# Performance work log

Hardware: AMD Instinct MI355X
Metric: run time of the kernel (lower is better)

## Reference

```python
import jax, jax.numpy as jnp
import numpy as np

GROUPS = 32
EPS = 1e-5
N_HEADS = 4


def group_norm(x, w, b):
    # x: [B, C, T]; GroupNorm over (C/G, T) within each of G groups
    B, C, T = x.shape
    xg = x.reshape(B, GROUPS, (C // GROUPS) * T)
    mean = xg.mean(axis=-1, keepdims=True)
    var = xg.var(axis=-1, keepdims=True)
    xn = ((xg - mean) * jax.lax.rsqrt(var + EPS)).reshape(B, C, T)
    return xn * w[None, :, None] + b[None, :, None]


def setup_inputs() -> dict:
    key = jax.random.key(0)
    ks = jax.random.split(key, 5)
    B, C, H, W = 2, 256, 64, 64
    x = jax.random.normal(ks[0], (B, C, H, W), dtype=jnp.float32)
    norm_w = jnp.ones((C,), dtype=jnp.float32)
    norm_b = jnp.zeros((C,), dtype=jnp.float32)
    qkv_w = jax.random.normal(ks[1], (3 * C, C), dtype=jnp.float32) * (C ** -0.5)
    qkv_b = jax.random.normal(ks[2], (3 * C,), dtype=jnp.float32) * 0.02
    proj_w = jax.random.normal(ks[3], (C, C), dtype=jnp.float32) * (C ** -0.5)
    proj_b = jax.random.normal(ks[4], (C,), dtype=jnp.float32) * 0.02
    return {"x": x, "norm_w": norm_w, "norm_b": norm_b,
            "qkv_w": qkv_w, "qkv_b": qkv_b,
            "proj_w": proj_w, "proj_b": proj_b}


def reference(x, norm_w, norm_b, qkv_w, qkv_b, proj_w, proj_b):
    B, C, Hs, Ws = x.shape
    T = Hs * Ws
    xf = x.reshape(B, C, T)
    xn = group_norm(xf, norm_w, norm_b)
    # 1x1 conv1d == channel matmul: [3C,C] x [B,C,T] -> [B,3C,T]
    qkv = jnp.einsum('oc,bct->bot', qkv_w, xn) + qkv_b[None, :, None]
    ch = C // N_HEADS
    # legacy order: [B, H*3*ch, T] -> [B*H, 3*ch, T] -> split
    qkv_h = qkv.reshape(B * N_HEADS, 3 * ch, T)
    q, k, v = qkv_h[:, :ch], qkv_h[:, ch:2 * ch], qkv_h[:, 2 * ch:]
    scale = ch ** -0.25
    # full [B*H, T, T] score matrix, softmax in fp32 (faithful to source)
    weight = jnp.einsum('bct,bcs->bts', q * scale, k * scale)
    weight = jax.nn.softmax(weight.astype(jnp.float32), axis=-1).astype(qkv.dtype)
    a = jnp.einsum('bts,bcs->bct', weight, v).reshape(B, C, T)
    h = jnp.einsum('oc,bct->bot', proj_w, a) + proj_b[None, :, None]
    return (xf + h).reshape(B, C, Hs, Ws)
```

## Files before the change

kernel.cpp:

```cpp
#include <hip/hip_runtime.h>
#include <hip/hip_bf16.h>

#define B_    2
#define C_    256
#define T_    4096
#define GRP   32
#define CPG   8
#define NH    4
#define CH    64
#define K3C   768
#define SPLIT 4
#define GSL   8
#define NSTAT (B_ * GRP * GSL)
#define NCVT  128
#define LOG2E 1.4426950408889634f

typedef __attribute__((ext_vector_type(8))) short bf16x8;
typedef __attribute__((ext_vector_type(4))) float f32x4;
typedef __attribute__((ext_vector_type(16))) float f32x16;

#if __has_builtin(__builtin_amdgcn_exp2f)
#define EXP2(x) __builtin_amdgcn_exp2f(x)
#else
#define EXP2(x) exp2f(x)
#endif

__device__ __forceinline__ unsigned pk2(float a, float b) {
    __hip_bfloat162 h = __float22bfloat162_rn(make_float2(a, b));
    union { __hip_bfloat162 h2; unsigned u; } cv; cv.h2 = h;
    return cv.u;
}
__device__ __forceinline__ float bf2f(unsigned short u) {
    return __uint_as_float((unsigned)u << 16);
}

__device__ __forceinline__ void gl_lds16(const unsigned short* g, unsigned short* l) {
    __builtin_amdgcn_global_load_lds(
        (const __attribute__((address_space(1))) unsigned int*)g,
        (__attribute__((address_space(3))) unsigned int*)l,
        16, 0, 0);
}

__global__ __launch_bounds__(256) void pre_kernel(
    const float* __restrict__ x, float* __restrict__ stat,
    const float* __restrict__ qw, const float* __restrict__ pw,
    unsigned short* __restrict__ qwb, unsigned short* __restrict__ pwb) {
    int bid = blockIdx.x;
    int tid = threadIdx.x;
    if (bid < NSTAT) {
        int bg = bid >> 3, sl = bid & 7;
        const int SLN = CPG * T_ / GSL;
        const float* xp = x + (size_t)bg * CPG * T_ + (size_t)sl * SLN;
        float s = 0.f, s2 = 0.f;
        for (int i = tid * 4; i < SLN; i += 1024) {
            float4 v = *(const float4*)&xp[i];
            s  += (v.x + v.y) + (v.z + v.w);
            s2 += (v.x * v.x + v.y * v.y) + (v.z * v.z + v.w * v.w);
        }
        for (int off = 32; off > 0; off >>= 1) {
            s  += __shfl_down(s,  off);
            s2 += __shfl_down(s2, off);
        }
        __shared__ float rs[4], rs2[4];
        int wid = tid >> 6;
        if ((tid & 63) == 0) { rs[wid] = s; rs2[wid] = s2; }
        __syncthreads();
        if (tid == 0) {
            stat[bid * 2]     = (rs[0] + rs[1]) + (rs[2] + rs[3]);
            stat[bid * 2 + 1] = (rs2[0] + rs2[1]) + (rs2[2] + rs2[3]);
        }
    } else {
        int i = (bid - NSTAT) * 256 + tid;
        const int n1 = K3C * C_ / 8;
        const float* src; unsigned short* dst;
        if (i < n1) { src = qw + 8 * i; dst = qwb + 8 * i; }
        else { int j = i - n1; src = pw + 8 * j; dst = pwb + 8 * j; }
        float4 a = *(const float4*)src;
        float4 b = *(const float4*)(src + 4);
        uint4 u;
        u.x = pk2(a.x, a.y); u.y = pk2(a.z, a.w);
        u.z = pk2(b.x, b.y); u.w = pk2(b.z, b.w);
        *(uint4*)dst = u;
    }
}

__global__ __launch_bounds__(256) void gn_apply_kernel(
    const float* __restrict__ x, const float* __restrict__ stat,
    const float* __restrict__ w, const float* __restrict__ b,
    unsigned short* __restrict__ xnT) {
    int bg = blockIdx.x, sl = blockIdx.y;
    int batch = bg / GRP, g = bg % GRP;
    const float* xp = x + (size_t)bg * CPG * T_;
    int tid = threadIdx.x;

    float s = 0.f, s2 = 0.f;
#pragma unroll
    for (int i = 0; i < GSL; ++i) {
        s  += stat[(bg * GSL + i) * 2];
        s2 += stat[(bg * GSL + i) * 2 + 1];
    }
    float inv_n = 1.f / (float)(CPG * T_);
    float mean = s * inv_n;
    float var  = s2 * inv_n - mean * mean;
    float inv  = rsqrtf(var + 1e-5f);

    float wv[8], bv[8];
#pragma unroll
    for (int j = 0; j < 8; j++) {
        float ww = w[g * CPG + j] * inv;
        wv[j] = ww;
        bv[j] = b[g * CPG + j] - mean * ww;
    }
    unsigned short* op = xnT + (size_t)batch * T_ * C_ + g * CPG;
    int t0 = sl * (T_ / GSL);
#pragma unroll
    for (int rep = 0; rep < 2; ++rep) {
        int t = t0 + rep * 256 + tid;
        float v[8];
#pragma unroll
        for (int j = 0; j < 8; j++) v[j] = xp[(size_t)j * T_ + t] * wv[j] + bv[j];
        uint4 u;
        u.x = pk2(v[0], v[1]); u.y = pk2(v[2], v[3]);
        u.z = pk2(v[4], v[5]); u.w = pk2(v[6], v[7]);
        *(uint4*)&op[(size_t)t * C_] = u;
    }
}

__global__ __launch_bounds__(256) void qkv_gemm_kernel(
    const unsigned short* __restrict__ Wb, const float* __restrict__ bias,
    const unsigned short* __restrict__ Xt, unsigned short* __restrict__ q_t,
    unsigned short* __restrict__ k_t, unsigned short* __restrict__ v_d) {
    int tb = blockIdx.x * 128;
    int by = blockIdx.y;
    int bz = blockIdx.z;
    int ob = by * 64;
    int tid = threadIdx.x;
    int l = tid & 15, oct = (tid >> 4) & 3, w = tid >> 6;

    __shared__ __align__(16) unsigned short SH[64 * 264];

#pragma unroll
    for (int j = 0; j < 8; ++j) {
        int idx = tid + 256 * j;
        int row = idx >> 5, ch = idx & 31;
        *(uint4*)&SH[row * 264 + ch * 8] =
            *(const uint4*)&Wb[(size_t)(ob + row) * C_ + ch * 8];
    }
    __syncthreads();

    const unsigned short* Xb = Xt + (size_t)bz * T_ * C_;

    f32x4 acc[4][2];
#pragma unroll
    for (int mf = 0; mf < 4; ++mf)
#pragma unroll
        for (int nf = 0; nf < 2; ++nf) acc[mf][nf] = (f32x4){0.f, 0.f, 0.f, 0.f};

#pragma unroll
    for (int kk = 0; kk < 8; ++kk) {
        int c0 = 32 * kk + 8 * oct;
        bf16x8 bfr[2];
#pragma unroll
        for (int nf = 0; nf < 2; ++nf)
            bfr[nf] = *(const bf16x8*)&Xb[(size_t)(tb + 32 * w + 16 * nf + l) * C_ + c0];
#pragma unroll
        for (int mf = 0; mf < 4; ++mf) {
            bf16x8 af = *(const bf16x8*)&SH[(16 * mf + l) * 264 + c0];
#pragma unroll
            for (int nf = 0; nf < 2; ++nf)
                acc[mf][nf] = __builtin_amdgcn_mfma_f32_16x16x32_bf16(af, bfr[nf], acc[mf][nf], 0, 0, 0);
        }
    }

    int head = by / 3, sec = by - 3 * head;
    int bh = bz * NH + head;

    if (sec < 2) {
        float scale = (sec == 0) ? 0.125f * LOG2E : 1.f;
        unsigned short* dst = ((sec == 0) ? q_t : k_t) + (size_t)bh * T_ * CH;
#pragma unroll
        for (int mf = 0; mf < 4; ++mf) {
            float bvs[4];
#pragma unroll
            for (int r = 0; r < 4; ++r) bvs[r] = bias[ob + 16 * mf + 4 * oct + r];
#pragma unroll
            for (int nf = 0; nf < 2; ++nf) {
                int t = tb + 32 * w + 16 * nf + l;
                float v0 = (acc[mf][nf][0] + bvs[0]) * scale;
                float v1 = (acc[mf][nf][1] + bvs[1]) * scale;
                float v2 = (acc[mf][nf][2] + bvs[2]) * scale;
                float v3 = (acc[mf][nf][3] + bvs[3]) * scale;
                uint2 u; u.x = pk2(v0, v1); u.y = pk2(v2, v3);
                *(uint2*)&dst[(size_t)t * CH + 16 * mf + 4 * oct] = u;
            }
        }
    } else {
        __syncthreads();
#pragma unroll
        for (int mf = 0; mf < 4; ++mf) {
            float bvs[4];
#pragma unroll
            for (int r = 0; r < 4; ++r) bvs[r] = bias[ob + 16 * mf + 4 * oct + r];
#pragma unroll
            for (int nf = 0; nf < 2; ++nf) {
                int tl = 32 * w + 16 * nf + l;
#pragma unroll
                for (int r = 0; r < 4; ++r) {
                    unsigned pv = pk2(acc[mf][nf][r] + bvs[r], 0.f);
                    SH[(16 * mf + 4 * oct + r) * 136 + tl] = (unsigned short)(pv & 0xffffu);
                }
            }
        }
        __syncthreads();
        unsigned short* vdst = v_d + (size_t)bh * CH * T_;
#pragma unroll
        for (int j = 0; j < 4; ++j) {
            int idx = tid + 256 * j;
            int row = idx >> 4, ch = idx & 15;
            *(uint4*)&vdst[(size_t)row * T_ + tb + ch * 8] =
                *(uint4*)&SH[row * 136 + ch * 8];
        }
    }
}

__global__ __launch_bounds__(256, 4) void attn_kernel(
    const unsigned short* __restrict__ q_t, const unsigned short* __restrict__ k_t,
    const unsigned short* __restrict__ v_d, unsigned short* __restrict__ Opart,
    float* __restrict__ lbuf) {
    int bh = blockIdx.y;
    int sp = blockIdx.z;
    int t0 = blockIdx.x * 128;
    int tid = threadIdx.x;
    int ln = tid & 63;
    int li = ln & 31;
    int hi = ln >> 5;
    int w  = tid >> 6;
    int l7 = li & 7;

    __shared__ __align__(16) unsigned short Kt[2][64 * 64];
    __shared__ __align__(16) unsigned short Vt[2][64 * 64];

    const unsigned short* qb = q_t + (size_t)bh * T_ * CH;
    const unsigned short* kb = k_t + (size_t)bh * T_ * CH;
    const unsigned short* vb = v_d + (size_t)bh * CH * T_;

    int tq = t0 + 32 * w + li;
    bf16x8 qf[4];
#pragma unroll
    for (int ks = 0; ks < 4; ++ks)
        qf[ks] = *(const bf16x8*)&qb[(size_t)tq * CH + ks * 16 + 8 * hi];

    int rsub = ln >> 3;
    int sch  = ln & 7;
    int cm8 = (sch ^ rsub) * 8;
    int kr0 = 16 * w + rsub;

#define STAGE(buf, s0) do {                                                          \
    gl_lds16(kb + (size_t)((s0) + kr0) * CH + cm8,     &Kt[buf][(16 * w) * 64]);     \
    gl_lds16(kb + (size_t)((s0) + kr0 + 8) * CH + cm8, &Kt[buf][(16 * w + 8) * 64]); \
    gl_lds16(vb + (size_t)kr0 * T_ + (s0) + cm8,       &Vt[buf][(16 * w) * 64]);     \
    gl_lds16(vb + (size_t)(kr0 + 8) * T_ + (s0) + cm8, &Vt[buf][(16 * w + 8) * 64]); \
} while (0)

    f32x16 O0, O1;
#pragma unroll
    for (int i = 0; i < 16; ++i) { O0[i] = 0.f; O1[i] = 0.f; }
    float l_run = 0.f;

    int s_beg = sp * (T_ / SPLIT);
    const int NT = (T_ / SPLIT) / 64;

    STAGE(0, s_beg);
    __syncthreads();

    int cur = 0;
    for (int t = 0; t < NT; ++t) {
        if (t + 1 < NT) STAGE(cur ^ 1, s_beg + (t + 1) * 64);

        f32x16 S0, S1;
#pragma unroll
        for (int i = 0; i < 16; ++i) { S0[i] = 0.f; S1[i] = 0.f; }
        __builtin_amdgcn_s_setprio(1);
#pragma unroll
        for (int ks = 0; ks < 4; ++ks) {
            bf16x8 ka0 = *(const bf16x8*)
                &Kt[cur][li * 64 + (((2 * ks + hi) ^ l7) * 8)];
            bf16x8 ka1 = *(const bf16x8*)
                &Kt[cur][(32 + li) * 64 + (((2 * ks + hi) ^ l7) * 8)];
            S0 = __builtin_amdgcn_mfma_f32_32x32x16_bf16(ka0, qf[ks], S0, 0, 0, 0);
            S1 = __builtin_amdgcn_mfma_f32_32x32x16_bf16(ka1, qf[ks], S1, 0, 0, 0);
        }
        __builtin_amdgcn_s_setprio(0);

        unsigned W0[8], W1[8];
        float lloc = 0.f;
#pragma unroll
        for (int h = 0; h < 4; ++h) {
            float a0 = EXP2(S0[4 * h + 0]), a1 = EXP2(S0[4 * h + 1]);
            float a2 = EXP2(S0[4 * h + 2]), a3 = EXP2(S0[4 * h + 3]);
            float b0 = EXP2(S1[4 * h + 0]), b1 = EXP2(S1[4 * h + 1]);
            float b2 = EXP2(S1[4 * h + 2]), b3 = EXP2(S1[4 * h + 3]);
            lloc += ((a0 + a1) + (a2 + a3)) + ((b0 + b1) + (b2 + b3));
            W0[2 * h] = pk2(a0, a1); W0[2 * h + 1] = pk2(a2, a3);
            W1[2 * h] = pk2(b0, b1); W1[2 * h + 1] = pk2(b2, b3);
        }
        l_run += lloc;

        __builtin_amdgcn_s_setprio(1);
#pragma unroll
        for (int g = 0; g < 4; ++g) {
            int ks = g & 1;
            unsigned w0, w1, w2, w3;
            if (g < 2) {
                w0 = W0[4 * ks + 0]; w1 = W0[4 * ks + 1];
                w2 = W0[4 * ks + 2]; w3 = W0[4 * ks + 3];
            } else {
                w0 = W1[4 * ks + 0]; w1 = W1[4 * ks + 1];
                w2 = W1[4 * ks + 2]; w3 = W1[4 * ks + 3];
            }
            asm("v_permlane32_swap_b32 %0, %1" : "+v"(w0), "+v"(w2));
            asm("v_permlane32_swap_b32 %0, %1" : "+v"(w1), "+v"(w3));
            union { unsigned u[4]; bf16x8 v; } pu;
            pu.u[0] = w0; pu.u[1] = w1; pu.u[2] = w2; pu.u[3] = w3;
            bf16x8 va0 = *(const bf16x8*)
                &Vt[cur][li * 64 + (((2 * g + hi) ^ l7) * 8)];
            bf16x8 va1 = *(const bf16x8*)
                &Vt[cur][(32 + li) * 64 + (((2 * g + hi) ^ l7) * 8)];
            O0 = __builtin_amdgcn_mfma_f32_32x32x16_bf16(va0, pu.v, O0, 0, 0, 0);
            O1 = __builtin_amdgcn_mfma_f32_32x32x16_bf16(va1, pu.v, O1, 0, 0, 0);
        }
        __builtin_amdgcn_s_setprio(0);

        __syncthreads();
        cur ^= 1;
    }
#undef STAGE

    float lt = l_run + __shfl_xor(l_run, 32);
    float inv = 1.f / lt;
    size_t row = (size_t)(sp * 8 + bh) * T_ + tq;
    unsigned short* op = Opart + row * CH;
#pragma unroll
    for (int cb = 0; cb < 2; ++cb) {
#pragma unroll
        for (int h = 0; h < 4; ++h) {
            int c = 32 * cb + 8 * h + 4 * hi;
            float v0, v1, v2, v3;
            if (cb == 0) {
                v0 = O0[4 * h + 0]; v1 = O0[4 * h + 1];
                v2 = O0[4 * h + 2]; v3 = O0[4 * h + 3];
            } else {
                v0 = O1[4 * h + 0]; v1 = O1[4 * h + 1];
                v2 = O1[4 * h + 2]; v3 = O1[4 * h + 3];
            }
            uint2 u;
            u.x = pk2(v0 * inv, v1 * inv);
            u.y = pk2(v2 * inv, v3 * inv);
            *(uint2*)&op[c] = u;
        }
    }
    if (hi == 0) lbuf[row] = lt;
}

__global__ __launch_bounds__(256) void proj_gemm_kernel(
    const unsigned short* __restrict__ Wb, const float* __restrict__ bias,
    const unsigned short* __restrict__ Opart, const float* __restrict__ lbuf,
    const float* __restrict__ xres, float* __restrict__ out) {
    int tb = blockIdx.x * 64;
    int ob = blockIdx.y * 64;
    int bz = blockIdx.z;
    int tid = threadIdx.x;
    int l = tid & 15, oct = (tid >> 4) & 3, w = tid >> 6;

    __shared__ __align__(16) unsigned short SH[64 * 264];

#pragma unroll
    for (int j = 0; j < 8; ++j) {
        int idx = tid + 256 * j;
        int row = idx >> 5, ch = idx & 31;
        *(uint4*)&SH[row * 264 + ch * 8] =
            *(const uint4*)&Wb[(size_t)(ob + row) * C_ + ch * 8];
    }
    __syncthreads();

    int t = tb + 16 * w + l;

    float lwn[SPLIT][NH];
#pragma unroll
    for (int h = 0; h < NH; ++h) {
        float lw[SPLIT], lsum = 0.f;
#pragma unroll
        for (int sp = 0; sp < SPLIT; ++sp) {
            lw[sp] = lbuf[(size_t)(sp * 8 + bz * NH + h) * T_ + t];
            lsum += lw[sp];
        }
        float inv = 1.f / lsum;
#pragma unroll
        for (int sp = 0; sp < SPLIT; ++sp) lwn[sp][h] = lw[sp] * inv;
    }

    f32x4 acc[4];
#pragma unroll
    for (int mf = 0; mf < 4; ++mf) acc[mf] = (f32x4){0.f, 0.f, 0.f, 0.f};

#pragma unroll
    for (int kk = 0; kk < 8; ++kk) {
        int c0 = 32 * kk + 8 * oct;
        int h  = kk >> 1;
        int cc = 32 * (kk & 1) + 8 * oct;

        float o[8];
#pragma unroll
        for (int j = 0; j < 8; ++j) o[j] = 0.f;
#pragma unroll
        for (int sp = 0; sp < SPLIT; ++sp) {
            const unsigned short* p =
                Opart + ((size_t)(sp * 8 + bz * NH + h) * T_ + t) * CH + cc;
            uint4 u = *(const uint4*)p;
            float s = lwn[sp][h];
            o[0] += bf2f((unsigned short)(u.x & 0xffffu)) * s;
            o[1] += bf2f((unsigned short)(u.x >> 16)) * s;
            o[2] += bf2f((unsigned short)(u.y & 0xffffu)) * s;
            o[3] += bf2f((unsigned short)(u.y >> 16)) * s;
            o[4] += bf2f((unsigned short)(u.z & 0xffffu)) * s;
            o[5] += bf2f((unsigned short)(u.z >> 16)) * s;
            o[6] += bf2f((unsigned short)(u.w & 0xffffu)) * s;
            o[7] += bf2f((unsigned short)(u.w >> 16)) * s;
        }
        union { uint4 u; bf16x8 v; } pb;
        pb.u.x = pk2(o[0], o[1]); pb.u.y = pk2(o[2], o[3]);
        pb.u.z = pk2(o[4], o[5]); pb.u.w = pk2(o[6], o[7]);

#pragma unroll
        for (int mf = 0; mf < 4; ++mf) {
            bf16x8 af = *(const bf16x8*)&SH[(16 * mf + l) * 264 + c0];
            acc[mf] = __builtin_amdgcn_mfma_f32_16x16x32_bf16(af, pb.v, acc[mf], 0, 0, 0);
        }
    }

#pragma unroll
    for (int mf = 0; mf < 4; ++mf) {
#pragma unroll
        for (int r = 0; r < 4; ++r) {
            int o = ob + 16 * mf + 4 * oct + r;
            size_t idx = ((size_t)bz * C_ + o) * T_ + t;
            out[idx] = acc[mf][r] + bias[o] + xres[idx];
        }
    }
}

extern "C" void kernel_launch(void* const* d_in, const int* in_sizes, int n_in,
                              void* d_out, int out_size, void* d_ws, size_t ws_size,
                              hipStream_t stream) {
    const float* x      = (const float*)d_in[0];
    const float* norm_w = (const float*)d_in[1];
    const float* norm_b = (const float*)d_in[2];
    const float* qkv_w  = (const float*)d_in[3];
    const float* qkv_b  = (const float*)d_in[4];
    const float* proj_w = (const float*)d_in[5];
    const float* proj_b = (const float*)d_in[6];
    float* out = (float*)d_out;

    char* p = (char*)d_ws;
    unsigned short* xnT = (unsigned short*)p; p += (size_t)B_ * T_ * C_ * 2;
    unsigned short* qwb = (unsigned short*)p; p += (size_t)K3C * C_ * 2;
    unsigned short* pwb = (unsigned short*)p; p += (size_t)C_ * C_ * 2;
    unsigned short* q_t = (unsigned short*)p; p += (size_t)B_ * NH * T_ * CH * 2;
    unsigned short* k_t = (unsigned short*)p; p += (size_t)B_ * NH * T_ * CH * 2;
    unsigned short* v_d = (unsigned short*)p; p += (size_t)B_ * NH * T_ * CH * 2;
    unsigned short* Opart = (unsigned short*)p; p += (size_t)SPLIT * 8 * T_ * CH * 2;
    float* lbuf         = (float*)p;          p += (size_t)SPLIT * 8 * T_ * 4;
    float* stat         = (float*)p;          p += (size_t)NSTAT * 2 * 4;

    pre_kernel<<<dim3(NSTAT + NCVT), dim3(256), 0, stream>>>(
        x, stat, qkv_w, proj_w, qwb, pwb);
    gn_apply_kernel<<<dim3(B_ * GRP, GSL), dim3(256), 0, stream>>>(
        x, stat, norm_w, norm_b, xnT);
    qkv_gemm_kernel<<<dim3(T_ / 128, 12, B_), dim3(256), 0, stream>>>(
        qwb, qkv_b, xnT, q_t, k_t, v_d);
    attn_kernel<<<dim3(T_ / 128, B_ * NH, SPLIT), dim3(256), 0, stream>>>(
        q_t, k_t, v_d, Opart, lbuf);
    proj_gemm_kernel<<<dim3(T_ / 64, C_ / 64, B_), dim3(256), 0, stream>>>(
        pwb, proj_b, Opart, lbuf, x, out);
}
```

Baseline: 146.7 us.

## Load K tiles directly into registers and interleave S0/S1 softmax

K fragments are no longer staged through LDS. Each wave loads its K operands straight from global memory into registers and prefetches the next tile's fragments after each QK MFMA half. The S0 and S1 score blocks are computed and exponentiated in sequence so the exp work on one half can overlap the MFMAs of the other, and the V LDS swizzle gains an extra XOR term to reduce bank conflicts. This halves LDS traffic and footprint, but every wave redundantly reads the same K rows from global or L2, and register pressure rises under the 4-block launch bound.

```diff
diff --git a/kernel.cpp b/kernel.cpp
--- a/kernel.cpp
+++ b/kernel.cpp
@@ -236,8 +236,8 @@
     int hi = ln >> 5;
     int w  = tid >> 6;
     int l7 = li & 7;
-
-    __shared__ __align__(16) unsigned short Kt[2][64 * 64];
+    int sw = l7 ^ ((li >> 3) & 3);
+
     __shared__ __align__(16) unsigned short Vt[2][64 * 64];
 
     const unsigned short* qb = q_t + (size_t)bh * T_ * CH;
@@ -252,14 +252,13 @@
 
     int rsub = ln >> 3;
     int sch  = ln & 7;
-    int cm8 = (sch ^ rsub) * 8;
-    int kr0 = 16 * w + rsub;
-
-#define STAGE(buf, s0) do {                                                          \
-    gl_lds16(kb + (size_t)((s0) + kr0) * CH + cm8,     &Kt[buf][(16 * w) * 64]);     \
-    gl_lds16(kb + (size_t)((s0) + kr0 + 8) * CH + cm8, &Kt[buf][(16 * w + 8) * 64]); \
-    gl_lds16(vb + (size_t)kr0 * T_ + (s0) + cm8,       &Vt[buf][(16 * w) * 64]);     \
-    gl_lds16(vb + (size_t)(kr0 + 8) * T_ + (s0) + cm8, &Vt[buf][(16 * w + 8) * 64]); \
+    int cm8_0 = (sch ^ rsub ^ ((2 * w) & 3)) * 8;
+    int cm8_1 = (sch ^ rsub ^ ((2 * w + 1) & 3)) * 8;
+    int vr0 = 16 * w + rsub;
+
+#define STAGE_V(buf, s0) do {                                                      \
+    gl_lds16(vb + (size_t)vr0 * T_ + (s0) + cm8_0,       &Vt[buf][(16 * w) * 64]);     \
+    gl_lds16(vb + (size_t)(vr0 + 8) * T_ + (s0) + cm8_1, &Vt[buf][(16 * w + 8) * 64]); \
 } while (0)
 
     f32x16 O0, O1;
@@ -270,38 +269,70 @@
     int s_beg = sp * (T_ / SPLIT);
     const int NT = (T_ / SPLIT) / 64;
 
-    STAGE(0, s_beg);
+    const unsigned short* kp = kb + ((size_t)s_beg + li) * CH + 8 * hi;
+    bf16x8 k0[4], k1[4];
+#pragma unroll
+    for (int ks = 0; ks < 4; ++ks) {
+        k0[ks] = *(const bf16x8*)(kp + ks * 16);
+        k1[ks] = *(const bf16x8*)(kp + 32 * CH + ks * 16);
+    }
+
+    STAGE_V(0, s_beg);
     __syncthreads();
 
     int cur = 0;
     for (int t = 0; t < NT; ++t) {
-        if (t + 1 < NT) STAGE(cur ^ 1, s_beg + (t + 1) * 64);
-
-        f32x16 S0, S1;
-#pragma unroll
-        for (int i = 0; i < 16; ++i) { S0[i] = 0.f; S1[i] = 0.f; }
+        int s0n = s_beg + (t + 1) * 64;
+        bool more = (t + 1 < NT);
+        if (more) STAGE_V(cur ^ 1, s0n);
+
+        f32x16 S0;
+#pragma unroll
+        for (int i = 0; i < 16; ++i) S0[i] = 0.f;
         __builtin_amdgcn_s_setprio(1);
 #pragma unroll
-        for (int ks = 0; ks < 4; ++ks) {
-            bf16x8 ka0 = *(const bf16x8*)
-                &Kt[cur][li * 64 + (((2 * ks + hi) ^ l7) * 8)];
-            bf16x8 ka1 = *(const bf16x8*)
-                &Kt[cur][(32 + li) * 64 + (((2 * ks + hi) ^ l7) * 8)];
-            S0 = __builtin_amdgcn_mfma_f32_32x32x16_bf16(ka0, qf[ks], S0, 0, 0, 0);
-            S1 = __builtin_amdgcn_mfma_f32_32x32x16_bf16(ka1, qf[ks], S1, 0, 0, 0);
-        }
+        for (int ks = 0; ks < 4; ++ks)
+            S0 = __builtin_amdgcn_mfma_f32_32x32x16_bf16(k0[ks], qf[ks], S0, 0, 0, 0);
         __builtin_amdgcn_s_setprio(0);
-
-        unsigned W0[8], W1[8];
+        if (more) {
+            const unsigned short* kpn = kp + 64 * CH;
+#pragma unroll
+            for (int ks = 0; ks < 4; ++ks)
+                k0[ks] = *(const bf16x8*)(kpn + ks * 16);
+        }
+
+        unsigned W0[8];
         float lloc = 0.f;
 #pragma unroll
         for (int h = 0; h < 4; ++h) {
             float a0 = EXP2(S0[4 * h + 0]), a1 = EXP2(S0[4 * h + 1]);
             float a2 = EXP2(S0[4 * h + 2]), a3 = EXP2(S0[4 * h + 3]);
+            lloc += (a0 + a1) + (a2 + a3);
+            W0[2 * h] = pk2(a0, a1); W0[2 * h + 1] = pk2(a2, a3);
+        }
+
+        f32x16 S1;
+#pragma unroll
+        for (int i = 0; i < 16; ++i) S1[i] = 0.f;
+        __builtin_amdgcn_s_setprio(1);
+#pragma unroll
+        for (int ks = 0; ks < 4; ++ks)
+            S1 = __builtin_amdgcn_mfma_f32_32x32x16_bf16(k1[ks], qf[ks], S1, 0, 0, 0);
+        __builtin_amdgcn_s_setprio(0);
+        if (more) {
+            const unsigned short* kpn = kp + 64 * CH;
+#pragma unroll
+            for (int ks = 0; ks < 4; ++ks)
+                k1[ks] = *(const bf16x8*)(kpn + 32 * CH + ks * 16);
+            kp = kpn;
+        }
+
+        unsigned W1[8];
+#pragma unroll
+        for (int h = 0; h < 4; ++h) {
             float b0 = EXP2(S1[4 * h + 0]), b1 = EXP2(S1[4 * h + 1]);
             float b2 = EXP2(S1[4 * h + 2]), b3 = EXP2(S1[4 * h + 3]);
-            lloc += ((a0 + a1) + (a2 + a3)) + ((b0 + b1) + (b2 + b3));
-            W0[2 * h] = pk2(a0, a1); W0[2 * h + 1] = pk2(a2, a3);
+            lloc += (b0 + b1) + (b2 + b3);
             W1[2 * h] = pk2(b0, b1); W1[2 * h + 1] = pk2(b2, b3);
         }
         l_run += lloc;
@@ -323,9 +354,9 @@
             union { unsigned u[4]; bf16x8 v; } pu;
             pu.u[0] = w0; pu.u[1] = w1; pu.u[2] = w2; pu.u[3] = w3;
             bf16x8 va0 = *(const bf16x8*)
-                &Vt[cur][li * 64 + (((2 * g + hi) ^ l7) * 8)];
+                &Vt[cur][li * 64 + (((2 * g + hi) ^ sw) * 8)];
             bf16x8 va1 = *(const bf16x8*)
-                &Vt[cur][(32 + li) * 64 + (((2 * g + hi) ^ l7) * 8)];
+                &Vt[cur][(32 + li) * 64 + (((2 * g + hi) ^ sw) * 8)];
             O0 = __builtin_amdgcn_mfma_f32_32x32x16_bf16(va0, pu.v, O0, 0, 0, 0);
             O1 = __builtin_amdgcn_mfma_f32_32x32x16_bf16(va1, pu.v, O1, 0, 0, 0);
         }
@@ -334,7 +365,7 @@
         __syncthreads();
         cur ^= 1;
     }
-#undef STAGE
+#undef STAGE_V
 
     float lt = l_run + __shfl_xor(l_run, 32);
     float inv = 1.f / lt;
```

New measurement: 174.2 us. 18.7% more time.

## Tile xnT and Opart into MFMA-fragment blocks and refine attention LDS swizzle

Applied to the files above, without the earlier changes.

Stores the normalized activations and the attention partial outputs in a blocked layout of 16 time steps by 8 channels, so each 16-lane MFMA operand fetch in the QKV and projection GEMMs reads one contiguous 256-byte chunk instead of strided rows. The attention kernel's K/V LDS swizzle also mixes row bits 3-4 into the XOR pattern, aiming to remove remaining bank conflicts on the 32x32 fragment reads. Producer and consumer indexing must stay in exact agreement, and the scattered stores in the producers may coalesce less well.

```diff
diff --git a/kernel.cpp b/kernel.cpp
--- a/kernel.cpp
+++ b/kernel.cpp
@@ -40,6 +40,7 @@
         (__attribute__((address_space(3))) unsigned int*)l,
         16, 0, 0);
 }
+
 
 __global__ __launch_bounds__(256) void pre_kernel(
     const float* __restrict__ x, float* __restrict__ stat,
@@ -111,7 +112,6 @@
         wv[j] = ww;
         bv[j] = b[g * CPG + j] - mean * ww;
     }
-    unsigned short* op = xnT + (size_t)batch * T_ * C_ + g * CPG;
     int t0 = sl * (T_ / GSL);
 #pragma unroll
     for (int rep = 0; rep < 2; ++rep) {
@@ -122,7 +122,8 @@
         uint4 u;
         u.x = pk2(v[0], v[1]); u.y = pk2(v[2], v[3]);
         u.z = pk2(v[4], v[5]); u.w = pk2(v[6], v[7]);
-        *(uint4*)&op[(size_t)t * C_] = u;
+        *(uint4*)&xnT[(((size_t)batch * 256 + (t >> 4)) * 32 + g) * 128
+                      + (t & 15) * 8] = u;
     }
 }
 
@@ -148,8 +149,6 @@
     }
     __syncthreads();
 
-    const unsigned short* Xb = Xt + (size_t)bz * T_ * C_;
-
     f32x4 acc[4][2];
 #pragma unroll
     for (int mf = 0; mf < 4; ++mf)
@@ -162,7 +161,9 @@
         bf16x8 bfr[2];
 #pragma unroll
         for (int nf = 0; nf < 2; ++nf)
-            bfr[nf] = *(const bf16x8*)&Xb[(size_t)(tb + 32 * w + 16 * nf + l) * C_ + c0];
+            bfr[nf] = *(const bf16x8*)
+                &Xt[(((size_t)bz * 256 + (tb >> 4) + 2 * w + nf) * 32
+                     + 4 * kk + oct) * 128 + l * 8];
 #pragma unroll
         for (int mf = 0; mf < 4; ++mf) {
             bf16x8 af = *(const bf16x8*)&SH[(16 * mf + l) * 264 + c0];
@@ -236,6 +237,7 @@
     int hi = ln >> 5;
     int w  = tid >> 6;
     int l7 = li & 7;
+    int sw = l7 ^ ((li >> 3) & 3);
 
     __shared__ __align__(16) unsigned short Kt[2][64 * 64];
     __shared__ __align__(16) unsigned short Vt[2][64 * 64];
@@ -252,14 +254,15 @@
 
     int rsub = ln >> 3;
     int sch  = ln & 7;
-    int cm8 = (sch ^ rsub) * 8;
+    int cm8_0 = (sch ^ rsub ^ ((2 * w) & 3)) * 8;
+    int cm8_1 = (sch ^ rsub ^ ((2 * w + 1) & 3)) * 8;
     int kr0 = 16 * w + rsub;
 
-#define STAGE(buf, s0) do {                                                          \
-    gl_lds16(kb + (size_t)((s0) + kr0) * CH + cm8,     &Kt[buf][(16 * w) * 64]);     \
-    gl_lds16(kb + (size_t)((s0) + kr0 + 8) * CH + cm8, &Kt[buf][(16 * w + 8) * 64]); \
-    gl_lds16(vb + (size_t)kr0 * T_ + (s0) + cm8,       &Vt[buf][(16 * w) * 64]);     \
-    gl_lds16(vb + (size_t)(kr0 + 8) * T_ + (s0) + cm8, &Vt[buf][(16 * w + 8) * 64]); \
+#define STAGE(buf, s0) do {                                                            \
+    gl_lds16(kb + (size_t)((s0) + kr0) * CH + cm8_0,     &Kt[buf][(16 * w) * 64]);     \
+    gl_lds16(kb + (size_t)((s0) + kr0 + 8) * CH + cm8_1, &Kt[buf][(16 * w + 8) * 64]); \
+    gl_lds16(vb + (size_t)kr0 * T_ + (s0) + cm8_0,       &Vt[buf][(16 * w) * 64]);     \
+    gl_lds16(vb + (size_t)(kr0 + 8) * T_ + (s0) + cm8_1, &Vt[buf][(16 * w + 8) * 64]); \
 } while (0)
 
     f32x16 O0, O1;
@@ -284,9 +287,9 @@
 #pragma unroll
         for (int ks = 0; ks < 4; ++ks) {
             bf16x8 ka0 = *(const bf16x8*)
-                &Kt[cur][li * 64 + (((2 * ks + hi) ^ l7) * 8)];
+                &Kt[cur][li * 64 + (((2 * ks + hi) ^ sw) * 8)];
             bf16x8 ka1 = *(const bf16x8*)
-                &Kt[cur][(32 + li) * 64 + (((2 * ks + hi) ^ l7) * 8)];
+                &Kt[cur][(32 + li) * 64 + (((2 * ks + hi) ^ sw) * 8)];
             S0 = __builtin_amdgcn_mfma_f32_32x32x16_bf16(ka0, qf[ks], S0, 0, 0, 0);
             S1 = __builtin_amdgcn_mfma_f32_32x32x16_bf16(ka1, qf[ks], S1, 0, 0, 0);
         }
@@ -323,9 +326,9 @@
             union { unsigned u[4]; bf16x8 v; } pu;
             pu.u[0] = w0; pu.u[1] = w1; pu.u[2] = w2; pu.u[3] = w3;
             bf16x8 va0 = *(const bf16x8*)
-                &Vt[cur][li * 64 + (((2 * g + hi) ^ l7) * 8)];
+                &Vt[cur][li * 64 + (((2 * g + hi) ^ sw) * 8)];
             bf16x8 va1 = *(const bf16x8*)
-                &Vt[cur][(32 + li) * 64 + (((2 * g + hi) ^ l7) * 8)];
+                &Vt[cur][(32 + li) * 64 + (((2 * g + hi) ^ sw) * 8)];
             O0 = __builtin_amdgcn_mfma_f32_32x32x16_bf16(va0, pu.v, O0, 0, 0, 0);
             O1 = __builtin_amdgcn_mfma_f32_32x32x16_bf16(va1, pu.v, O1, 0, 0, 0);
         }
@@ -338,13 +341,12 @@
 
     float lt = l_run + __shfl_xor(l_run, 32);
     float inv = 1.f / lt;
-    size_t row = (size_t)(sp * 8 + bh) * T_ + tq;
-    unsigned short* op = Opart + row * CH;
+    size_t obase = ((size_t)(sp * 8 + bh) * 256 + (tq >> 4)) * 8;
+    int ti = tq & 15;
 #pragma unroll
     for (int cb = 0; cb < 2; ++cb) {
 #pragma unroll
         for (int h = 0; h < 4; ++h) {
-            int c = 32 * cb + 8 * h + 4 * hi;
             float v0, v1, v2, v3;
             if (cb == 0) {
                 v0 = O0[4 * h + 0]; v1 = O0[4 * h + 1];
@@ -356,10 +358,10 @@
             uint2 u;
             u.x = pk2(v0 * inv, v1 * inv);
             u.y = pk2(v2 * inv, v3 * inv);
-            *(uint2*)&op[c] = u;
-        }
-    }
-    if (hi == 0) lbuf[row] = lt;
+            *(uint2*)&Opart[(obase + 4 * cb + h) * 128 + ti * 8 + 4 * hi] = u;
+        }
+    }
+    if (hi == 0) lbuf[(size_t)(sp * 8 + bh) * T_ + tq] = lt;
 }
 
 __global__ __launch_bounds__(256) void proj_gemm_kernel(
@@ -407,15 +409,16 @@
     for (int kk = 0; kk < 8; ++kk) {
         int c0 = 32 * kk + 8 * oct;
         int h  = kk >> 1;
-        int cc = 32 * (kk & 1) + 8 * oct;
+        int cc = 4 * (kk & 1) + oct;
 
         float o[8];
 #pragma unroll
         for (int j = 0; j < 8; ++j) o[j] = 0.f;
 #pragma unroll
         for (int sp = 0; sp < SPLIT; ++sp) {
-            const unsigned short* p =
-                Opart + ((size_t)(sp * 8 + bz * NH + h) * T_ + t) * CH + cc;
+            const unsigned short* p = Opart +
+                (((size_t)(sp * 8 + bz * NH + h) * 256 + (t >> 4)) * 8 + cc) * 128
+                + (t & 15) * 8;
             uint4 u = *(const uint4*)p;
             float s = lwn[sp][h];
             o[0] += bf2f((unsigned short)(u.x & 0xffffu)) * s;
```

Measured after the change: 135.5 us. 7.6% less time.
